# Performance work log

Hardware: AMD Instinct MI355X
Metric: run time of the kernel (lower is better)

The kernel has to match this reference:

```python
import jax, jax.numpy as jnp
import numpy as np

B, T_CTX, N_EMBD, N_ATTN, N_HEAD = 8, 1024, 1024, 1024, 16
HEAD_SIZE = N_ATTN // N_HEAD


def _init_time_w():
    # replicates the torch init: per-head exponential decay curves
    curve = np.array([-(T_CTX - 1 - i) for i in range(T_CTX)], dtype=np.float64)
    ww = np.ones((N_HEAD, T_CTX), dtype=np.float32)
    for h in range(N_HEAD):
        if h < N_HEAD - 1:
            decay_speed = T_CTX ** (-(h + 1) / (N_HEAD - 1))
        else:
            decay_speed = 0.0
        ww[h] = np.exp(curve * decay_speed).astype(np.float32)
    return jnp.asarray(ww)


def setup_inputs() -> dict:
    key = jax.random.key(0)
    ks = jax.random.split(key, 6)
    s = 0.02
    return {
        "x": jax.random.normal(ks[0], (B, T_CTX, N_EMBD), jnp.float32),
        "time_w": _init_time_w(),                                   # [H, TT]
        "time_alpha": jnp.ones((N_HEAD, 1, T_CTX), jnp.float32),
        "time_beta": jnp.ones((N_HEAD, T_CTX, 1), jnp.float32),
        "time_gamma": jnp.ones((T_CTX, 1), jnp.float32),
        "Wk": jax.random.normal(ks[1], (N_ATTN, N_EMBD), jnp.float32) * s,
        "bk": jnp.zeros((N_ATTN,), jnp.float32),
        "Wv": jax.random.normal(ks[2], (N_ATTN, N_EMBD), jnp.float32) * s,
        "bv": jnp.zeros((N_ATTN,), jnp.float32),
        "Wr": jax.random.normal(ks[3], (N_ATTN, N_EMBD), jnp.float32) * s,
        "br": jnp.zeros((N_ATTN,), jnp.float32),
        "Wo": jax.random.normal(ks[4], (N_EMBD, N_ATTN), jnp.float32) * s,
        "bo": jnp.zeros((N_EMBD,), jnp.float32),
    }


def _build_w(time_w, time_alpha, time_beta, T):
    # w[h,t,u] = time_w[h, TT-1-(t-u)] for u<=t else 0  (causal decay matrix)
    TT = time_w.shape[1]
    t = jnp.arange(T)[:, None]
    u = jnp.arange(T)[None, :]
    idx = jnp.clip((TT - 1) - t + u, 0, TT - 1)
    mask = u <= t
    w = jnp.where(mask[None, :, :], time_w[:, idx], 0.0)  # [H, T, T]
    return w * time_alpha[:, :, :T] * time_beta[:, :T, :]


def reference(x, time_w, time_alpha, time_beta, time_gamma,
              Wk, bk, Wv, bv, Wr, br, Wo, bo):
    Bb, T, C = x.shape
    H = time_w.shape[0]
    w = _build_w(time_w, time_alpha, time_beta, T)  # [H,T,T]

    # time shift on the first half of channels: prepend zero row, drop last
    x_half = jnp.pad(x[:, :, : C // 2], ((0, 0), (1, 0), (0, 0)))[:, :T, :]
    xs = jnp.concatenate([x_half, x[:, :, C // 2 :]], axis=-1)

    k = xs @ Wk.T + bk
    v = xs @ Wv.T + bv
    r = xs @ Wr.T + br

    k = jnp.exp(jnp.clip(k, -60.0, 30.0))
    sum_k = jnp.cumsum(k, axis=1)  # [B,T,NA]

    kv = (k * v).reshape(Bb, T, H, -1)               # [B,T,H,hs]
    wkv = jnp.einsum('htu,buhc->bthc', w, kv).reshape(Bb, T, -1)

    rwkv = jax.nn.sigmoid(r) * wkv / sum_k
    out = rwkv @ Wo.T + bo
    return out * time_gamma[:T]
```

## Files before the change

### kernel.cpp

```cpp
#include <hip/hip_runtime.h>
#include <hip/hip_bf16.h>
#include <cstddef>
#include <cstdint>

#define B_SZ   8
#define T_CTX  1024
#define C_DIM  1024
#define H_NUM  16
#define HS     64
#define M_ROWS (B_SZ * T_CTX)

typedef __attribute__((ext_vector_type(8))) short bf16x8;
typedef __attribute__((ext_vector_type(8))) unsigned short u16x8;
typedef __attribute__((ext_vector_type(4))) float f32x4;

static __device__ inline unsigned short f2bf(float f) {
    __hip_bfloat16 h = __float2bfloat16(f);
    return __builtin_bit_cast(unsigned short, h);
}
static __device__ inline float bf2f(unsigned short u) {
    unsigned int v = ((unsigned int)u) << 16;
    return __builtin_bit_cast(float, v);
}
static __device__ inline void gld16(const void* g, void* l) {
    __builtin_amdgcn_global_load_lds((const __attribute__((address_space(1))) void*)g,
                                     (__attribute__((address_space(3))) void*)l,
                                     16, 0, 0);
}

__global__ __launch_bounds__(256)
void convert_all(const float* __restrict__ x, unsigned short* __restrict__ xs,
                 const float* __restrict__ Wk, const float* __restrict__ Wv,
                 const float* __restrict__ Wr, const float* __restrict__ Wo,
                 unsigned short* __restrict__ wdst)
{
    const int bid = blockIdx.x;
    if (bid < 8192) {
        const int idx = (bid * 256 + threadIdx.x) * 4;
        const int m = idx >> 10;
        const int c = idx & 1023;
        float4 v;
        if (c < 512) {
            const int t = m & (T_CTX - 1);
            if (t == 0) v = make_float4(0.f, 0.f, 0.f, 0.f);
            else        v = *(const float4*)(x + (size_t)(m - 1) * C_DIM + c);
        } else {
            v = *(const float4*)(x + idx);
        }
        ushort4 o;
        o.x = f2bf(v.x); o.y = f2bf(v.y); o.z = f2bf(v.z); o.w = f2bf(v.w);
        *(ushort4*)(xs + idx) = o;
    } else {
        const int wid = bid - 8192;
        const int z = wid >> 10;
        const float* src = (z == 0) ? Wk : (z == 1) ? Wv : (z == 2) ? Wr : Wo;
        const int idx = ((wid & 1023) * 256 + threadIdx.x) * 4;
        const float4 v = *(const float4*)(src + idx);
        ushort4 o;
        o.x = f2bf(v.x); o.y = f2bf(v.y); o.z = f2bf(v.z); o.w = f2bf(v.w);
        *(ushort4*)(wdst + (size_t)z * (C_DIM * C_DIM) + idx) = o;
    }
}

__global__ __launch_bounds__(256, 2)
void mfma_gemm64(const unsigned short* __restrict__ A,
                 const unsigned short* __restrict__ Wb,
                 const float* __restrict__ b0, const float* __restrict__ b1,
                 const float* __restrict__ b2,
                 void* __restrict__ o0, void* __restrict__ o1, void* __restrict__ o2,
                 const float* __restrict__ gamma, int multi)
{
    const int d  = blockIdx.x;
    const int y  = ((d & 7) << 3) | ((d >> 3) & 7);
    const int xb = d >> 6;
    const int m0 = y * 128, n0 = xb * 128;

    int mode, ncol0;
    const float* bias;
    void* out;
    if (multi) {
        const int z = n0 >> 10;
        mode = z;
        ncol0 = n0 & 1023;
        bias = (z == 0) ? b0 : (z == 1) ? b1 : b2;
        out  = (z == 0) ? o0 : (z == 1) ? o1 : o2;
    } else {
        mode = 3; ncol0 = n0; bias = b0; out = o0;
    }

    __shared__ unsigned short As[128 * 64];
    __shared__ unsigned short Bs[128 * 64];

    const int tid = threadIdx.x;
    const int w = tid >> 6, l = tid & 63;

    const int r8  = l >> 3;
    const int c16 = ((l & 7) ^ r8) * 8;
    const unsigned short* gA = A  + (size_t)(m0 + w * 32 + r8) * C_DIM + c16;
    const unsigned short* gB = Wb + (size_t)(n0 + w * 32 + r8) * C_DIM + c16;
    char* lA = (char*)As + (w * 32) * 128;
    char* lB = (char*)Bs + (w * 32) * 128;

    const int wr = w >> 1, wc = w & 1;
    const int lr = l & 15, lkq = l >> 4;
    const int x7 = lr & 7;

    f32x4 acc[4][4];
    #pragma unroll
    for (int i = 0; i < 4; ++i)
        #pragma unroll
        for (int j = 0; j < 4; ++j) acc[i][j] = (f32x4){0.f, 0.f, 0.f, 0.f};

    for (int k0 = 0; k0 < C_DIM; k0 += 64) {
        #pragma unroll
        for (int r = 0; r < 4; ++r) {
            gld16(gA + k0 + (size_t)r * 8 * C_DIM, lA + r * 8 * 128);
            gld16(gB + k0 + (size_t)r * 8 * C_DIM, lB + r * 8 * 128);
        }
        __syncthreads();

        bf16x8 af[2][4], bfv[2][4];
        #pragma unroll
        for (int ks = 0; ks < 2; ++ks) {
            const int slot = ((ks * 4 + lkq) ^ x7) * 8;
            #pragma unroll
            for (int i = 0; i < 4; ++i)
                af[ks][i] = *(const bf16x8*)&As[(wr * 64 + i * 16 + lr) * 64 + slot];
            #pragma unroll
            for (int j = 0; j < 4; ++j)
                bfv[ks][j] = *(const bf16x8*)&Bs[(wc * 64 + j * 16 + lr) * 64 + slot];
        }
        #pragma unroll
        for (int ks = 0; ks < 2; ++ks)
            #pragma unroll
            for (int i = 0; i < 4; ++i)
                #pragma unroll
                for (int j = 0; j < 4; ++j)
                    acc[i][j] = __builtin_amdgcn_mfma_f32_16x16x32_bf16(
                        af[ks][i], bfv[ks][j], acc[i][j], 0, 0, 0);
        __syncthreads();
    }

    #pragma unroll
    for (int j = 0; j < 4; ++j) {
        const int col = ncol0 + wc * 64 + j * 16 + lr;
        const float bz = bias[col];
        #pragma unroll
        for (int i = 0; i < 4; ++i) {
            const int rb = m0 + wr * 64 + i * 16 + lkq * 4;
            #pragma unroll
            for (int r = 0; r < 4; ++r) {
                const int row = rb + r;
                float v = acc[i][j][r] + bz;
                if (mode == 0)      v = __expf(fminf(fmaxf(v, -60.f), 30.f));
                else if (mode == 2) v = 1.f / (1.f + __expf(-v));
                else if (mode == 3) v *= gamma[row & (T_CTX - 1)];
                if (mode == 1 || mode == 2)
                    ((unsigned short*)out)[(size_t)row * C_DIM + col] = f2bf(v);
                else
                    ((float*)out)[(size_t)row * C_DIM + col] = v;
            }
        }
    }
}

__global__ __launch_bounds__(256)
void cumsum_chunk(const float* __restrict__ expk, const unsigned short* __restrict__ vbf,
                  const float* __restrict__ alpha,
                  float* __restrict__ sumk, unsigned short* __restrict__ kvT,
                  float* __restrict__ aux)
{
    const int n = blockIdx.x * 256 + threadIdx.x;
    const int q = blockIdx.y;
    const int b = blockIdx.z;
    const int h = n >> 6, c = n & 63;
    const size_t base = ((size_t)b * T_CTX + q * 128) * C_DIM + n;
    unsigned short* kvrow = kvT + (((size_t)b * H_NUM + h) * HS + c) * T_CTX + q * 128;
    float s = 0.f;
    u16x8 buf;
    for (int i = 0; i < 128; ++i) {
        const size_t idx = base + (size_t)i * C_DIM;
        const float e  = expk[idx];
        const float vv = bf2f(vbf[idx]);
        const float a  = alpha[h * T_CTX + q * 128 + i];
        s += e;
        sumk[idx] = s;
        buf[i & 7] = f2bf(e * vv * a);
        if ((i & 7) == 7) *(u16x8*)(kvrow + i - 7) = buf;
    }
    aux[((size_t)b * 8 + q) * C_DIM + n] = s;
}

#define REPL_STRIDE 1176
#define REPL_USED   1168

__global__ __launch_bounds__(256)
void wkv_mfma(const unsigned short* __restrict__ kvT,
              const float* __restrict__ sumk,
              const unsigned short* __restrict__ sigr,
              const float* __restrict__ tw, const float* __restrict__ beta,
              const float* __restrict__ aux,
              unsigned short* __restrict__ rwkv)
{
    __shared__ unsigned short repl[8 * REPL_STRIDE];
    __shared__ unsigned short kv_s[64 * 72];
    __shared__ unsigned short tw_s[1024];

    const int tid = threadIdx.x;
    const int bx = blockIdx.x;
    const int t0 = bx * 128;
    const int h  = blockIdx.y;
    const int b  = blockIdx.z;

    {
        const int i = tid * 4;
        const float4 v = *(const float4*)(tw + h * T_CTX + i);
        ushort4 o;
        o.x = f2bf(v.x); o.y = f2bf(v.y); o.z = f2bf(v.z); o.w = f2bf(v.w);
        *(ushort4*)&tw_s[i] = o;
    }
    __syncthreads();

    #pragma unroll
    for (int r = 0; r < 8; ++r)
        for (int i = tid; i < REPL_USED; i += 256) {
            const int src = i + r;
            repl[r * REPL_STRIDE + i] = (src < 1024) ? tw_s[src] : (unsigned short)0;
        }
    __syncthreads();

    const int w = tid >> 6, l = tid & 63;
    const int wr = w >> 1, wc = w & 1;
    const int lr = l & 15, lkq = l >> 4;

    const int r    = (7 - lr) & 7;
    const int S0   = 1023 - t0 - wr * 64 - lr + lkq * 8;
    const int abase = 2 * S0 + (2 * REPL_STRIDE - 2) * r;
    const char* repl_c = (const char*)repl;

    const int srow = tid >> 2;
    const int ucol = (tid & 3) * 16;
    const unsigned short* gkv = kvT + (((size_t)b * H_NUM + h) * HS + srow) * T_CTX + ucol;
    unsigned short* skv = &kv_s[srow * 72 + ucol];

    f32x4 acc[4][2];
    #pragma unroll
    for (int i = 0; i < 4; ++i) {
        acc[i][0] = (f32x4){0.f, 0.f, 0.f, 0.f};
        acc[i][1] = (f32x4){0.f, 0.f, 0.f, 0.f};
    }

    const int nsteps = t0 / 64 + 2;
    for (int ks = 0; ks < nsteps; ++ks) {
        const int u0 = ks * 64;
        const u16x8 q0 = *(const u16x8*)(gkv + u0);
        const u16x8 q1 = *(const u16x8*)(gkv + u0 + 8);
        __syncthreads();
        *(u16x8*)skv       = q0;
        *(u16x8*)(skv + 8) = q1;
        __syncthreads();

        const int ub = abase + 2 * u0;
        #pragma unroll
        for (int kk = 0; kk < 2; ++kk) {
            bf16x8 af[4], bfv[2];
            #pragma unroll
            for (int i = 0; i < 4; ++i)
                af[i] = *(const bf16x8*)(repl_c + (ub + kk * 64 - i * 32));
            #pragma unroll
            for (int j = 0; j < 2; ++j)
                bfv[j] = *(const bf16x8*)&kv_s[(wc * 32 + j * 16 + lr) * 72 + kk * 32 + lkq * 8];
            #pragma unroll
            for (int i = 0; i < 4; ++i)
                #pragma unroll
                for (int j = 0; j < 2; ++j)
                    acc[i][j] = __builtin_amdgcn_mfma_f32_16x16x32_bf16(
                        af[i], bfv[j], acc[i][j], 0, 0, 0);
        }
    }

    float off[2];
    #pragma unroll
    for (int j = 0; j < 2; ++j) {
        const int cl = wc * 32 + j * 16 + lr;
        float o = 0.f;
        for (int q = 0; q < bx; ++q)
            o += aux[((size_t)b * 8 + q) * C_DIM + h * HS + cl];
        off[j] = o;
    }

    #pragma unroll
    for (int i = 0; i < 4; ++i) {
        const int tb = t0 + wr * 64 + i * 16 + lkq * 4;
        #pragma unroll
        for (int rg = 0; rg < 4; ++rg) {
            const int t = tb + rg;
            const float bet = beta[h * T_CTX + t];
            const size_t row_off = ((size_t)(b * T_CTX + t)) * C_DIM + h * HS;
            #pragma unroll
            for (int j = 0; j < 2; ++j) {
                const int cl = wc * 32 + j * 16 + lr;
                const float sk = sumk[row_off + cl] + off[j];
                const float sr = bf2f(sigr[row_off + cl]);
                rwkv[row_off + cl] = f2bf(sr * bet * acc[i][j][rg] / sk);
            }
        }
    }
}

extern "C" void kernel_launch(void* const* d_in, const int* in_sizes, int n_in,
                              void* d_out, int out_size, void* d_ws, size_t ws_size,
                              hipStream_t stream)
{
    const float* x     = (const float*)d_in[0];
    const float* tw    = (const float*)d_in[1];
    const float* alpha = (const float*)d_in[2];
    const float* beta  = (const float*)d_in[3];
    const float* gamma = (const float*)d_in[4];
    const float* Wk    = (const float*)d_in[5];
    const float* bk    = (const float*)d_in[6];
    const float* Wv    = (const float*)d_in[7];
    const float* bv    = (const float*)d_in[8];
    const float* Wr    = (const float*)d_in[9];
    const float* br    = (const float*)d_in[10];
    const float* Wo    = (const float*)d_in[11];
    const float* bo    = (const float*)d_in[12];
    float* out = (float*)d_out;

    char* W = (char*)d_ws;
    float* expk          = (float*)W;
    unsigned short* rwkv = (unsigned short*)W;
    unsigned short* vbf  = (unsigned short*)(W + (32ull << 20));
    unsigned short* wbf  = (unsigned short*)(W + (48ull << 20));
    float* aux           = (float*)(W + (56ull << 20));
    float* sumk          = (float*)(W + (64ull << 20));
    unsigned short* xs   = (unsigned short*)(W + (64ull << 20));
    unsigned short* sigr = (unsigned short*)(W + (96ull << 20));
    unsigned short* kvT  = (unsigned short*)(W + (112ull << 20));

    const size_t WSZ = (size_t)C_DIM * C_DIM;

    convert_all<<<dim3(12288), 256, 0, stream>>>(x, xs, Wk, Wv, Wr, Wo, wbf);

    mfma_gemm64<<<dim3(1536), 256, 0, stream>>>(
        xs, wbf, bk, bv, br, expk, vbf, sigr, gamma, 1);

    cumsum_chunk<<<dim3(4, 8, 8), 256, 0, stream>>>(expk, vbf, alpha, sumk, kvT, aux);

    wkv_mfma<<<dim3(8, 16, 8), 256, 0, stream>>>(
        kvT, sumk, sigr, tw, beta, aux, rwkv);

    mfma_gemm64<<<dim3(512), 256, 0, stream>>>(
        rwkv, wbf + 3 * WSZ, bo, nullptr, nullptr,
        out, nullptr, nullptr, gamma, 0);
}
```

Baseline: 272.0 us.

## Triple-buffer GEMM with async LDS loads and 128x256 tiles over 512 threads

```diff
diff --git a/kernel.cpp b/kernel.cpp
--- a/kernel.cpp
+++ b/kernel.cpp
@@ -62,7 +62,7 @@
     }
 }
 
-__global__ __launch_bounds__(256, 2)
+__global__ __launch_bounds__(512, 2)
 void mfma_gemm64(const unsigned short* __restrict__ A,
                  const unsigned short* __restrict__ Wb,
                  const float* __restrict__ b0, const float* __restrict__ b1,
@@ -70,10 +70,13 @@
                  void* __restrict__ o0, void* __restrict__ o1, void* __restrict__ o2,
                  const float* __restrict__ gamma, int multi)
 {
-    const int d  = blockIdx.x;
-    const int y  = ((d & 7) << 3) | ((d >> 3) & 7);
-    const int xb = d >> 6;
-    const int m0 = y * 128, n0 = xb * 128;
+    const int d     = blockIdx.x;
+    const int ntn   = multi ? 12 : 4;
+    const int chunk = multi ? 96 : 32;
+    const int g  = (d & 7) * chunk + (d >> 3);
+    const int ty = g / ntn;
+    const int tx = g - ty * ntn;
+    const int m0 = ty * 128, n0 = tx * 256;
 
     int mode, ncol0;
     const float* bias;
@@ -88,22 +91,26 @@
         mode = 3; ncol0 = n0; bias = b0; out = o0;
     }
 
-    __shared__ unsigned short As[128 * 64];
-    __shared__ unsigned short Bs[128 * 64];
+    __shared__ unsigned short As[3][128 * 64];
+    __shared__ unsigned short Bs[3][256 * 64];
 
     const int tid = threadIdx.x;
     const int w = tid >> 6, l = tid & 63;
 
     const int r8  = l >> 3;
     const int c16 = ((l & 7) ^ r8) * 8;
-    const unsigned short* gA = A  + (size_t)(m0 + w * 32 + r8) * C_DIM + c16;
+    const unsigned short* gA = A  + (size_t)(m0 + w * 16 + r8) * C_DIM + c16;
     const unsigned short* gB = Wb + (size_t)(n0 + w * 32 + r8) * C_DIM + c16;
-    char* lA = (char*)As + (w * 32) * 128;
-    char* lB = (char*)Bs + (w * 32) * 128;
-
-    const int wr = w >> 1, wc = w & 1;
+    unsigned short* lA0 = &As[0][0] + w * 16 * 64;
+    unsigned short* lB0 = &Bs[0][0] + w * 32 * 64;
+
+    const int wr = w >> 2, wc = w & 3;
     const int lr = l & 15, lkq = l >> 4;
     const int x7 = lr & 7;
+    const int s0 = (lkq ^ x7) * 8;
+    const int s1 = s0 ^ 32;
+    const int arow = (wr * 64 + lr) * 64;
+    const int brow = (wc * 64 + lr) * 64;
 
     f32x4 acc[4][4];
     #pragma unroll
@@ -111,34 +118,64 @@
         #pragma unroll
         for (int j = 0; j < 4; ++j) acc[i][j] = (f32x4){0.f, 0.f, 0.f, 0.f};
 
-    for (int k0 = 0; k0 < C_DIM; k0 += 64) {
-        #pragma unroll
-        for (int r = 0; r < 4; ++r) {
-            gld16(gA + k0 + (size_t)r * 8 * C_DIM, lA + r * 8 * 128);
-            gld16(gB + k0 + (size_t)r * 8 * C_DIM, lB + r * 8 * 128);
-        }
-        __syncthreads();
-
-        bf16x8 af[2][4], bfv[2][4];
-        #pragma unroll
-        for (int ks = 0; ks < 2; ++ks) {
-            const int slot = ((ks * 4 + lkq) ^ x7) * 8;
-            #pragma unroll
-            for (int i = 0; i < 4; ++i)
-                af[ks][i] = *(const bf16x8*)&As[(wr * 64 + i * 16 + lr) * 64 + slot];
+    auto stage = [&](int kt, int buf) {
+        const unsigned short* ga = gA + kt * 64;
+        const unsigned short* gb = gB + kt * 64;
+        char* la = (char*)(lA0 + buf * (128 * 64));
+        char* lb = (char*)(lB0 + buf * (256 * 64));
+        gld16(ga,                      la);
+        gld16(ga + (size_t)8  * C_DIM, la + 8  * 128);
+        gld16(gb,                      lb);
+        gld16(gb + (size_t)8  * C_DIM, lb + 8  * 128);
+        gld16(gb + (size_t)16 * C_DIM, lb + 16 * 128);
+        gld16(gb + (size_t)24 * C_DIM, lb + 24 * 128);
+    };
+
+    stage(0, 0); stage(1, 1); stage(2, 2);
+
+    int cur = 0;
+    for (int kt = 0; kt < 16; ++kt) {
+        if (kt < 14)       asm volatile("s_waitcnt vmcnt(12)" ::: "memory");
+        else if (kt == 14) asm volatile("s_waitcnt vmcnt(6)"  ::: "memory");
+        else               asm volatile("s_waitcnt vmcnt(0)"  ::: "memory");
+        __builtin_amdgcn_s_barrier();
+        __builtin_amdgcn_sched_barrier(0);
+
+        const unsigned short* a_s = &As[cur][0];
+        const unsigned short* b_s = &Bs[cur][0];
+
+        bf16x8 af0[4], bv0[4], af1[4], bv1[4];
+        #pragma unroll
+        for (int i = 0; i < 4; ++i) af0[i] = *(const bf16x8*)&a_s[arow + i * 1024 + s0];
+        #pragma unroll
+        for (int j = 0; j < 4; ++j) bv0[j] = *(const bf16x8*)&b_s[brow + j * 1024 + s0];
+        __builtin_amdgcn_s_setprio(1);
+        #pragma unroll
+        for (int i = 0; i < 4; ++i)
             #pragma unroll
             for (int j = 0; j < 4; ++j)
-                bfv[ks][j] = *(const bf16x8*)&Bs[(wc * 64 + j * 16 + lr) * 64 + slot];
-        }
-        #pragma unroll
-        for (int ks = 0; ks < 2; ++ks)
-            #pragma unroll
-            for (int i = 0; i < 4; ++i)
-                #pragma unroll
-                for (int j = 0; j < 4; ++j)
-                    acc[i][j] = __builtin_amdgcn_mfma_f32_16x16x32_bf16(
-                        af[ks][i], bfv[ks][j], acc[i][j], 0, 0, 0);
-        __syncthreads();
+                acc[i][j] = __builtin_amdgcn_mfma_f32_16x16x32_bf16(
+                    af0[i], bv0[j], acc[i][j], 0, 0, 0);
+        __builtin_amdgcn_s_setprio(0);
+
+        #pragma unroll
+        for (int i = 0; i < 4; ++i) af1[i] = *(const bf16x8*)&a_s[arow + i * 1024 + s1];
+        #pragma unroll
+        for (int j = 0; j < 4; ++j) bv1[j] = *(const bf16x8*)&b_s[brow + j * 1024 + s1];
+        __builtin_amdgcn_s_setprio(1);
+        #pragma unroll
+        for (int i = 0; i < 4; ++i)
+            #pragma unroll
+            for (int j = 0; j < 4; ++j)
+                acc[i][j] = __builtin_amdgcn_mfma_f32_16x16x32_bf16(
+                    af1[i], bv1[j], acc[i][j], 0, 0, 0);
+        __builtin_amdgcn_s_setprio(0);
+
+        asm volatile("s_waitcnt lgkmcnt(0)" ::: "memory");
+        __builtin_amdgcn_s_barrier();
+        __builtin_amdgcn_sched_barrier(0);
+        if (kt < 13) stage(kt + 3, cur);
+        cur = (cur == 2) ? 0 : cur + 1;
     }
 
     #pragma unroll
@@ -342,7 +379,7 @@
 
     convert_all<<<dim3(12288), 256, 0, stream>>>(x, xs, Wk, Wv, Wr, Wo, wbf);
 
-    mfma_gemm64<<<dim3(1536), 256, 0, stream>>>(
+    mfma_gemm64<<<dim3(768), 512, 0, stream>>>(
         xs, wbf, bk, bv, br, expk, vbf, sigr, gamma, 1);
 
     cumsum_chunk<<<dim3(4, 8, 8), 256, 0, stream>>>(expk, vbf, alpha, sumk, kvT, aux);
@@ -350,7 +387,7 @@
     wkv_mfma<<<dim3(8, 16, 8), 256, 0, stream>>>(
         kvT, sumk, sigr, tw, beta, aux, rwkv);
 
-    mfma_gemm64<<<dim3(512), 256, 0, stream>>>(
+    mfma_gemm64<<<dim3(256), 512, 0, stream>>>(
         rwkv, wbf + 3 * WSZ, bo, nullptr, nullptr,
         out, nullptr, nullptr, gamma, 0);
 }
```

Result: slower. 296.9 us (+9.1%).

## Use 256x256-tile pipelined MFMA GEMM for fused K/V/R projection

Applied to the files above, without the earlier changes.

```diff
diff --git a/kernel.cpp b/kernel.cpp
--- a/kernel.cpp
+++ b/kernel.cpp
@@ -62,31 +62,163 @@
     }
 }
 
+__global__ __launch_bounds__(512, 2)
+void mfma_gemm256(const unsigned short* __restrict__ A,
+                  const unsigned short* __restrict__ Wb,
+                  const float* __restrict__ b0, const float* __restrict__ b1,
+                  const float* __restrict__ b2,
+                  void* __restrict__ o0, void* __restrict__ o1, void* __restrict__ o2)
+{
+    const int d = blockIdx.x;
+    const int g = (d & 7) * 48 + (d >> 3);
+    const int ty = g / 12, tx = g - ty * 12;
+    const int m0 = ty * 256, n0 = tx * 256;
+    const int z = n0 >> 10;
+    const int ncol0 = n0 & 1023;
+    const float* bias = (z == 0) ? b0 : (z == 1) ? b1 : b2;
+    void* out = (z == 0) ? o0 : (z == 1) ? o1 : o2;
+
+    __shared__ unsigned short Ash[4 * 8192];
+    __shared__ unsigned short Bsh[4 * 8192];
+
+    const int tid = threadIdx.x;
+    const int w = tid >> 6, l = tid & 63;
+
+    const int lrow = l >> 2;
+    const int lchk = (((l & 3) ^ ((l >> 3) & 3)) * 8);
+    const unsigned short* gAs = A  + (size_t)(m0 + w * 32 + lrow) * C_DIM + lchk;
+    const unsigned short* gBs = Wb + (size_t)(n0 + w * 32 + lrow) * C_DIM + lchk;
+    unsigned short* const dA = Ash + w * 1024;
+    unsigned short* const dB = Bsh + w * 1024;
+
+    auto stA = [&](int kt, int ks, int s) {
+        const unsigned short* p = gAs + kt * 64 + ks * 32;
+        gld16(p,              dA + s * 8192);
+        gld16(p + 16 * C_DIM, dA + s * 8192 + 512);
+    };
+    auto stB = [&](int kt, int ks, int s) {
+        const unsigned short* p = gBs + kt * 64 + ks * 32;
+        gld16(p,              dB + s * 8192);
+        gld16(p + 16 * C_DIM, dB + s * 8192 + 512);
+    };
+
+    const int wr = w >> 2, wc = w & 3;
+    const int lr = l & 15, lkq = l >> 4;
+    const int cw = (lkq ^ ((lr >> 1) & 3)) * 16;
+    const int abase = (wr * 128 + lr) * 64 + cw;
+    const int bbase = (wc * 64 + lr) * 64 + cw;
+    const char* const Ac = (const char*)Ash;
+    const char* const Bc = (const char*)Bsh;
+
+    bf16x8 af[4], bfr[4];
+    auto ldA = [&](int s, int oh) {
+        const char* base = Ac + s * 16384 + abase + oh * 4096;
+        af[0] = *(const bf16x8*)(base);
+        af[1] = *(const bf16x8*)(base + 1024);
+        af[2] = *(const bf16x8*)(base + 2048);
+        af[3] = *(const bf16x8*)(base + 3072);
+    };
+    auto ldB = [&](int s) {
+        const char* base = Bc + s * 16384 + bbase;
+        bfr[0] = *(const bf16x8*)(base);
+        bfr[1] = *(const bf16x8*)(base + 1024);
+        bfr[2] = *(const bf16x8*)(base + 2048);
+        bfr[3] = *(const bf16x8*)(base + 3072);
+    };
+
+    f32x4 acc[8][4];
+    #pragma unroll
+    for (int i = 0; i < 8; ++i)
+        #pragma unroll
+        for (int j = 0; j < 4; ++j) acc[i][j] = (f32x4){0.f, 0.f, 0.f, 0.f};
+
+    auto mm = [&](int mb) {
+        __builtin_amdgcn_s_setprio(1);
+        #pragma unroll
+        for (int mi = 0; mi < 4; ++mi)
+            #pragma unroll
+            for (int j = 0; j < 4; ++j)
+                acc[mb + mi][j] = __builtin_amdgcn_mfma_f32_16x16x32_bf16(
+                    af[mi], bfr[j], acc[mb + mi][j], 0, 0, 0);
+        __builtin_amdgcn_s_setprio(0);
+    };
+
+    stA(0, 0, 0); stB(0, 0, 0);
+    stA(0, 1, 1); stB(0, 1, 1);
+    stA(1, 0, 2); stB(1, 0, 2);
+
+    for (int kt = 0; kt < 16; ++kt) {
+        const int s0 = (2 * kt) & 3, s1 = (2 * kt + 1) & 3, sn = (2 * kt + 3) & 3;
+        if (kt < 15) asm volatile("s_waitcnt vmcnt(4)" ::: "memory");
+        else         asm volatile("s_waitcnt vmcnt(0)" ::: "memory");
+        __builtin_amdgcn_s_barrier();
+        __builtin_amdgcn_sched_barrier(0);
+        ldA(s0, 0); ldB(s0);
+        if (kt < 15) stA(kt + 1, 1, sn);
+        asm volatile("s_waitcnt lgkmcnt(0)" ::: "memory");
+        __builtin_amdgcn_sched_barrier(0);
+        mm(0);
+        __builtin_amdgcn_s_barrier();
+        __builtin_amdgcn_sched_barrier(0);
+        ldA(s0, 1);
+        if (kt < 15) stB(kt + 1, 1, sn);
+        asm volatile("s_waitcnt lgkmcnt(0)" ::: "memory");
+        __builtin_amdgcn_sched_barrier(0);
+        mm(4);
+        __builtin_amdgcn_s_barrier();
+        __builtin_amdgcn_sched_barrier(0);
+        ldA(s1, 0); ldB(s1);
+        if (kt < 14) stA(kt + 2, 0, s0);
+        asm volatile("s_waitcnt lgkmcnt(0)" ::: "memory");
+        __builtin_amdgcn_sched_barrier(0);
+        mm(0);
+        __builtin_amdgcn_s_barrier();
+        __builtin_amdgcn_sched_barrier(0);
+        ldA(s1, 1);
+        if (kt < 14) stB(kt + 2, 0, s0);
+        asm volatile("s_waitcnt lgkmcnt(0)" ::: "memory");
+        __builtin_amdgcn_sched_barrier(0);
+        mm(4);
+        __builtin_amdgcn_s_barrier();
+        __builtin_amdgcn_sched_barrier(0);
+    }
+
+    #pragma unroll
+    for (int j = 0; j < 4; ++j) {
+        const int col = ncol0 + wc * 64 + j * 16 + lr;
+        const float bz = bias[col];
+        #pragma unroll
+        for (int mi = 0; mi < 8; ++mi) {
+            const int rb = m0 + wr * 128 + mi * 16 + lkq * 4;
+            #pragma unroll
+            for (int r = 0; r < 4; ++r) {
+                const int row = rb + r;
+                float v = acc[mi][j][r] + bz;
+                if (z == 0) {
+                    v = __expf(fminf(fmaxf(v, -60.f), 30.f));
+                    ((float*)out)[(size_t)row * C_DIM + col] = v;
+                } else if (z == 2) {
+                    v = 1.f / (1.f + __expf(-v));
+                    ((unsigned short*)out)[(size_t)row * C_DIM + col] = f2bf(v);
+                } else {
+                    ((unsigned short*)out)[(size_t)row * C_DIM + col] = f2bf(v);
+                }
+            }
+        }
+    }
+}
+
 __global__ __launch_bounds__(256, 2)
 void mfma_gemm64(const unsigned short* __restrict__ A,
                  const unsigned short* __restrict__ Wb,
-                 const float* __restrict__ b0, const float* __restrict__ b1,
-                 const float* __restrict__ b2,
-                 void* __restrict__ o0, void* __restrict__ o1, void* __restrict__ o2,
-                 const float* __restrict__ gamma, int multi)
+                 const float* __restrict__ b0,
+                 void* __restrict__ o0,
+                 const float* __restrict__ gamma)
 {
     const int d  = blockIdx.x;
     const int y  = ((d & 7) << 3) | ((d >> 3) & 7);
     const int xb = d >> 6;
     const int m0 = y * 128, n0 = xb * 128;
-
-    int mode, ncol0;
-    const float* bias;
-    void* out;
-    if (multi) {
-        const int z = n0 >> 10;
-        mode = z;
-        ncol0 = n0 & 1023;
-        bias = (z == 0) ? b0 : (z == 1) ? b1 : b2;
-        out  = (z == 0) ? o0 : (z == 1) ? o1 : o2;
-    } else {
-        mode = 3; ncol0 = n0; bias = b0; out = o0;
-    }
 
     __shared__ unsigned short As[128 * 64];
     __shared__ unsigned short Bs[128 * 64];
@@ -143,22 +275,16 @@
 
     #pragma unroll
     for (int j = 0; j < 4; ++j) {
-        const int col = ncol0 + wc * 64 + j * 16 + lr;
-        const float bz = bias[col];
+        const int col = n0 + wc * 64 + j * 16 + lr;
+        const float bz = b0[col];
         #pragma unroll
         for (int i = 0; i < 4; ++i) {
             const int rb = m0 + wr * 64 + i * 16 + lkq * 4;
             #pragma unroll
             for (int r = 0; r < 4; ++r) {
                 const int row = rb + r;
-                float v = acc[i][j][r] + bz;
-                if (mode == 0)      v = __expf(fminf(fmaxf(v, -60.f), 30.f));
-                else if (mode == 2) v = 1.f / (1.f + __expf(-v));
-                else if (mode == 3) v *= gamma[row & (T_CTX - 1)];
-                if (mode == 1 || mode == 2)
-                    ((unsigned short*)out)[(size_t)row * C_DIM + col] = f2bf(v);
-                else
-                    ((float*)out)[(size_t)row * C_DIM + col] = v;
+                float v = (acc[i][j][r] + bz) * gamma[row & (T_CTX - 1)];
+                ((float*)o0)[(size_t)row * C_DIM + col] = v;
             }
         }
     }
@@ -342,8 +468,8 @@
 
     convert_all<<<dim3(12288), 256, 0, stream>>>(x, xs, Wk, Wv, Wr, Wo, wbf);
 
-    mfma_gemm64<<<dim3(1536), 256, 0, stream>>>(
-        xs, wbf, bk, bv, br, expk, vbf, sigr, gamma, 1);
+    mfma_gemm256<<<dim3(384), 512, 0, stream>>>(
+        xs, wbf, bk, bv, br, expk, vbf, sigr);
 
     cumsum_chunk<<<dim3(4, 8, 8), 256, 0, stream>>>(expk, vbf, alpha, sumk, kvT, aux);
 
@@ -351,6 +477,5 @@
         kvT, sumk, sigr, tw, beta, aux, rwkv);
 
     mfma_gemm64<<<dim3(512), 256, 0, stream>>>(
-        rwkv, wbf + 3 * WSZ, bo, nullptr, nullptr,
-        out, nullptr, nullptr, gamma, 0);
-}
+        rwkv, wbf + 3 * WSZ, bo, out, gamma);
+}
```

Measured after the change: 295.2 us. 8.5% more time.
